# Kernel tuning notes

Hardware: AMD Instinct MI355X
Metric: run time of the kernel (lower is better)

## Reference

```python
import jax, jax.numpy as jnp
from jax import lax
import numpy as np

WIDTH = 3.0        # tool half-width (voxels)
SIGMA = 1.0        # soft mask edge (voxels)
BLUR_SIGMA = 1.5   # post-deposit isotropic blur sigma (voxels)
EPS = 1e-8


def _gauss_blur(x, sigma):
    """Separable Gaussian blur over the last two axes of x: [B, X, Y]."""
    radius = int(3 * sigma)
    t = jnp.arange(-radius, radius + 1, dtype=x.dtype)
    k = jnp.exp(-0.5 * (t / sigma) ** 2)
    k = k / k.sum()
    x4 = x[:, None]                      # [B,1,X,Y] NCHW
    kh = k.reshape(1, 1, -1, 1)
    x4 = lax.conv_general_dilated(x4, kh, (1, 1), 'SAME')
    kw = k.reshape(1, 1, 1, -1)
    x4 = lax.conv_general_dilated(x4, kw, (1, 1), 'SAME')
    return x4[:, 0]


def setup_inputs() -> dict:
    key = jax.random.key(0)
    k1, k2, k3 = jax.random.split(key, 3)
    B, H, W = 16, 1024, 1024
    occ = jax.random.uniform(k1, (B, H, W), dtype=jnp.float32)
    # push start/end points well inside the grid (voxel coordinates)
    action_start = jax.random.uniform(k2, (B, 3), minval=200.0, maxval=800.0, dtype=jnp.float32)
    action_end = action_start + jax.random.uniform(k3, (B, 3), minval=-150.0, maxval=150.0, dtype=jnp.float32)
    return {"occ": occ, "action_start": action_start, "action_end": action_end}


def reference(occ, action_start, action_end):
    # coordinate-convention transpose (see SplatPushModel docs)
    rho = jnp.swapaxes(occ, 1, 2)            # [B, X, Y]
    B, X, Y = rho.shape
    p0 = action_start[:, :2]                 # [B,2]
    p1 = action_end[:, :2]                   # [B,2]

    d = p1 - p0
    L = jnp.sqrt(jnp.sum(d * d, axis=-1) + EPS)      # [B] segment length
    u = d / L[:, None]                               # unit push direction
    n = jnp.stack([-u[:, 1], u[:, 0]], axis=-1)      # unit normal

    gx = jnp.arange(X, dtype=rho.dtype)[None, :, None]   # [1,X,1]
    gy = jnp.arange(Y, dtype=rho.dtype)[None, None, :]   # [1,1,Y]
    bc = lambda v: v[:, None, None]                      # [B] -> [B,1,1]

    # --- swept band: soft distance-to-segment mask ---
    rx = gx - bc(p0[:, 0])
    ry = gy - bc(p0[:, 1])
    t = jnp.clip(rx * bc(u[:, 0]) + ry * bc(u[:, 1]), 0.0, L[:, None, None])
    dx = rx - t * bc(u[:, 0])
    dy = ry - t * bc(u[:, 1])
    dist = jnp.sqrt(dx * dx + dy * dy + EPS)
    swept = jax.nn.sigmoid((WIDTH - dist) / SIGMA)       # [B,X,Y]

    m_swept = jnp.sum(rho * swept, axis=(1, 2))          # [B] mass to move
    pile_depth = m_swept / (2.0 * WIDTH)                 # [B]

    # --- landing zone probe (rectangle past p1) ---
    qx = gx - bc(p1[:, 0])
    qy = gy - bc(p1[:, 1])
    s = qx * bc(u[:, 0]) + qy * bc(u[:, 1])              # along-direction coord
    r = qx * bc(n[:, 0]) + qy * bc(n[:, 1])              # perpendicular coord
    lat = jax.nn.sigmoid((WIDTH - jnp.abs(r)) / SIGMA)
    probe = jax.nn.sigmoid(s / SIGMA) * jax.nn.sigmoid((bc(pile_depth) - s) / SIGMA) * lat
    existing = jnp.sum(rho * probe, axis=(1, 2))         # [B]
    extra = existing / (2.0 * WIDTH)                     # [B] forward extension

    # --- deposit band, shifted forward by extra_depth ---
    dep_mask = (jax.nn.sigmoid((s - bc(extra)) / SIGMA)
                * jax.nn.sigmoid((bc(extra) + bc(pile_depth) - s) / SIGMA)
                * lat)
    dep_norm = m_swept / (jnp.sum(dep_mask, axis=(1, 2)) + EPS)
    dep = dep_mask * dep_norm[:, None, None]             # mass-conserving deposit

    if BLUR_SIGMA > 0:
        dep = _gauss_blur(dep, BLUR_SIGMA)

    rho_new = rho * (1.0 - swept) + dep
    return jnp.swapaxes(rho_new, 1, 2)
```

## Files before the change

kernel.cpp:

```cpp
#include <hip/hip_runtime.h>
#include <hip/hip_bf16.h>
#include <math.h>

#define BB    16
#define HH    1024
#define WW    1024
#define NPIX  (HH * WW)
#define EPSF  1e-8f
#define RAD   4
#define MARG  24.f
#define NB1   128
#define NB2   64

struct BlurK { float k[9]; };

__device__ __forceinline__ float sigf(float z) {
    z = fmaxf(fminf(z, 40.f), -40.f);
    return 1.f / (1.f + __expf(-z));
}

struct Geom { float p0x, p0y, p1x, p1y, L, ux, uy; };

__device__ __forceinline__ Geom load_geom(const float* as, const float* ae, int b) {
    Geom g;
    g.p0x = as[3 * b];  g.p0y = as[3 * b + 1];
    g.p1x = ae[3 * b];  g.p1y = ae[3 * b + 1];
    float dx = g.p1x - g.p0x, dy = g.p1y - g.p0y;
    g.L  = sqrtf(dx * dx + dy * dy + EPSF);
    g.ux = dx / g.L;  g.uy = dy / g.L;
    return g;
}

__device__ __forceinline__ float sweptf(const Geom& g, float x, float y) {
    float rx = x - g.p0x, ry = y - g.p0y;
    float t  = fminf(fmaxf(rx * g.ux + ry * g.uy, 0.f), g.L);
    float dx = rx - t * g.ux, dy = ry - t * g.uy;
    float dist = sqrtf(dx * dx + dy * dy + EPSF);
    return sigf(3.f - dist);
}

__device__ __forceinline__ void slat(const Geom& g, float x, float y, float& s, float& lat) {
    float qx = x - g.p1x, qy = y - g.p1y;
    s = qx * g.ux + qy * g.uy;
    float r = qx * (-g.uy) + qy * g.ux;
    lat = sigf(3.f - fabsf(r));
}

__device__ __forceinline__ void capsule_bbox(const Geom& g, float m,
                                             int& x0, int& x1, int& y0, int& y1) {
    x0 = max(0, (int)floorf(fminf(g.p0x, g.p1x) - m));
    x1 = min(WW - 1, (int)ceilf(fmaxf(g.p0x, g.p1x) + m));
    y0 = max(0, (int)floorf(fminf(g.p0y, g.p1y) - m));
    y1 = min(HH - 1, (int)ceilf(fmaxf(g.p0y, g.p1y) + m));
}

__device__ __forceinline__ void strip_bbox(const Geom& g, float s0, float s1, float m,
                                           int& x0, int& x1, int& y0, int& y1) {
    float xmin = 1e9f, xmax = -1e9f, ymin = 1e9f, ymax = -1e9f;
    #pragma unroll
    for (int i = 0; i < 4; i++) {
        float s = (i & 1) ? s1 : s0;
        float r = (i & 2) ? m : -m;
        float x = g.p1x + s * g.ux - r * g.uy;
        float y = g.p1y + s * g.uy + r * g.ux;
        xmin = fminf(xmin, x); xmax = fmaxf(xmax, x);
        ymin = fminf(ymin, y); ymax = fmaxf(ymax, y);
    }
    x0 = max(0, (int)floorf(xmin)); x1 = min(WW - 1, (int)ceilf(xmax));
    y0 = max(0, (int)floorf(ymin)); y1 = min(HH - 1, (int)ceilf(ymax));
}

__device__ __forceinline__ float brb256(float v, float* sm) {
    #pragma unroll
    for (int off = 32; off > 0; off >>= 1) v += __shfl_down(v, off);
    const int lane = threadIdx.x & 63, wid = threadIdx.x >> 6;
    if (lane == 0) sm[wid] = v;
    __syncthreads();
    float r = sm[0] + sm[1] + sm[2] + sm[3];
    __syncthreads();
    return r;
}

__global__ __launch_bounds__(256)
void k_copy_mswept(const float* __restrict__ occ, const float* __restrict__ as,
                   const float* __restrict__ ae, float* __restrict__ out,
                   float* __restrict__ part1) {
    const int b = blockIdx.y, bx = blockIdx.x, tid = threadIdx.x;
    const float4* src = (const float4*)(occ + ((size_t)b << 20));
    float4*       dst = (float4*)(out + ((size_t)b << 20));
    const int base4 = bx * 2048 + tid;
    float4 v[8];
    #pragma unroll
    for (int k = 0; k < 8; k++) v[k] = src[base4 + k * 256];
    #pragma unroll
    for (int k = 0; k < 8; k++) dst[base4 + k * 256] = v[k];

    Geom g = load_geom(as, ae, b);
    int cx0, cx1, cy0, cy1; capsule_bbox(g, MARG, cx0, cx1, cy0, cy1);
    const int x = tid << 2;
    float sum = 0.f;
    if (x + 3 >= cx0 && x <= cx1) {
        #pragma unroll
        for (int k = 0; k < 8; k++) {
            const int y = bx * 8 + k;
            if (y >= cy0 && y <= cy1) {
                float fy = (float)y, fx = (float)x;
                sum += v[k].x * sweptf(g, fx + 0.f, fy);
                sum += v[k].y * sweptf(g, fx + 1.f, fy);
                sum += v[k].z * sweptf(g, fx + 2.f, fy);
                sum += v[k].w * sweptf(g, fx + 3.f, fy);
            }
        }
    }
    __shared__ float sm[4];
    float bs = brb256(sum, sm);
    if (tid == 0) part1[b * NB1 + bx] = bs;
}

__global__ __launch_bounds__(256)
void k_existing(const float* __restrict__ occ, const float* __restrict__ as,
                const float* __restrict__ ae, const float* __restrict__ part1,
                float* __restrict__ part2) {
    const int b = blockIdx.y, bx = blockIdx.x, tid = threadIdx.x;
    __shared__ float sm[4];
    const float m_swept = brb256((tid < NB1) ? part1[b * NB1 + tid] : 0.f, sm);
    const float pile = m_swept * (1.f / 6.f);

    Geom g = load_geom(as, ae, b);
    int x0, x1, y0, y1; strip_bbox(g, -MARG, pile + MARG, MARG, x0, x1, y0, y1);
    const float* base = occ + ((size_t)b << 20);
    float sum = 0.f;
    for (int y = y0 + bx; y <= y1; y += NB2) {
        float fy = (float)y;
        for (int x = x0 + tid; x <= x1; x += 256) {
            float s, lat; slat(g, (float)x, fy, s, lat);
            sum += base[((size_t)y << 10) + x] * sigf(s) * sigf(pile - s) * lat;
        }
    }
    float bs = brb256(sum, sm);
    if (tid == 0) part2[b * NB2 + bx] = bs;
}

__global__ __launch_bounds__(256)
void k_summask(const float* __restrict__ as, const float* __restrict__ ae,
               const float* __restrict__ part1, const float* __restrict__ part2,
               float* __restrict__ part3) {
    const int b = blockIdx.y, bx = blockIdx.x, tid = threadIdx.x;
    __shared__ float sm[4];
    const float m_swept  = brb256((tid < NB1) ? part1[b * NB1 + tid] : 0.f, sm);
    const float existing = brb256((tid < NB2) ? part2[b * NB2 + tid] : 0.f, sm);
    const float pile  = m_swept * (1.f / 6.f);
    const float extra = existing * (1.f / 6.f);

    Geom g = load_geom(as, ae, b);
    int x0, x1, y0, y1; strip_bbox(g, extra - MARG, extra + pile + MARG, MARG, x0, x1, y0, y1);
    float sum = 0.f;
    for (int y = y0 + bx; y <= y1; y += NB2) {
        float fy = (float)y;
        for (int x = x0 + tid; x <= x1; x += 256) {
            float s, lat; slat(g, (float)x, fy, s, lat);
            sum += sigf(s - extra) * sigf(extra + pile - s) * lat;
        }
    }
    float bs = brb256(sum, sm);
    if (tid == 0) part3[b * NB2 + bx] = bs;
}

#define TH 8
#define TW 128
__global__ __launch_bounds__(256)
void k_patch(const float* __restrict__ occ, const float* __restrict__ as,
             const float* __restrict__ ae, const float* __restrict__ part1,
             const float* __restrict__ part2, const float* __restrict__ part3,
             float* __restrict__ out, BlurK wk) {
    const int b = blockIdx.y, bx = blockIdx.x, tid = threadIdx.x;
    __shared__ float sm[4];
    const float m_swept  = brb256((tid < NB1) ? part1[b * NB1 + tid] : 0.f, sm);
    const float existing = brb256((tid < NB2) ? part2[b * NB2 + tid] : 0.f, sm);
    const float summask  = brb256((tid < NB2) ? part3[b * NB2 + tid] : 0.f, sm);
    const float pile     = m_swept * (1.f / 6.f);
    const float extra    = existing * (1.f / 6.f);
    const float dep_norm = m_swept / (summask + EPSF);

    Geom g = load_geom(as, ae, b);
    int cx0, cx1, cy0, cy1; capsule_bbox(g, MARG, cx0, cx1, cy0, cy1);
    int sx0, sx1, sy0, sy1; strip_bbox(g, extra - MARG, extra + pile + MARG, MARG, sx0, sx1, sy0, sy1);
    const int ux0 = min(cx0, sx0), ux1 = max(cx1, sx1);
    const int uy0 = min(cy0, sy0), uy1 = max(cy1, sy1);
    const int bw = ux1 - ux0 + 1, bh = uy1 - uy0 + 1;
    const int ntx = (bw + TW - 1) / TW, nty = (bh + TH - 1) / TH;

    __shared__ float draw[TH + 2 * RAD][TW + 2 * RAD];
    __shared__ float hb[TH + 2 * RAD][TW];
    const float* ob = occ + ((size_t)b << 20);
    float* outb = out + ((size_t)b << 20);

    for (int t = bx; t < ntx * nty; t += NB2) {
        const int tx = t % ntx, ty = t / ntx;
        const int xt = ux0 + tx * TW, yt = uy0 + ty * TH;
        for (int i = tid; i < (TH + 8) * (TW + 8); i += 256) {
            int ly = i / (TW + 8), lx = i % (TW + 8);
            int gy = yt - RAD + ly, gx = xt - RAD + lx;
            float v = 0.f;
            if (gx >= 0 && gx < WW && gy >= 0 && gy < HH) {
                float s, lat; slat(g, (float)gx, (float)gy, s, lat);
                v = sigf(s - extra) * sigf(extra + pile - s) * lat * dep_norm;
            }
            draw[ly][lx] = v;
        }
        __syncthreads();
        for (int i = tid; i < (TH + 8) * TW; i += 256) {
            int ly = i / TW, lx = i % TW;
            float acc = 0.f;
            #pragma unroll
            for (int j = 0; j < 9; j++) acc += wk.k[j] * draw[ly][lx + j];
            hb[ly][lx] = acc;
        }
        __syncthreads();
        for (int i = tid; i < TH * TW; i += 256) {
            int ly = i / TW, lx = i % TW;
            int gy = yt + ly, gx = xt + lx;
            if (gy < HH && gx < WW) {
                float acc = 0.f;
                #pragma unroll
                for (int j = 0; j < 9; j++) acc += wk.k[j] * hb[ly + j][lx];
                size_t off = ((size_t)gy << 10) + gx;
                float o = ob[off];
                outb[off] = o * (1.f - sweptf(g, (float)gx, (float)gy)) + acc;
            }
        }
        __syncthreads();
    }
}

extern "C" void kernel_launch(void* const* d_in, const int* in_sizes, int n_in,
                              void* d_out, int out_size, void* d_ws, size_t ws_size,
                              hipStream_t stream) {
    const float* occ = (const float*)d_in[0];
    const float* as  = (const float*)d_in[1];
    const float* ae  = (const float*)d_in[2];
    float* out   = (float*)d_out;
    float* part1 = (float*)d_ws;
    float* part2 = part1 + BB * NB1;
    float* part3 = part2 + BB * NB2;

    BlurK wk;
    {
        float s = 0.f;
        for (int i = 0; i < 9; i++) {
            float t = (float)(i - RAD) / 1.5f;
            wk.k[i] = expf(-0.5f * t * t);
            s += wk.k[i];
        }
        for (int i = 0; i < 9; i++) wk.k[i] /= s;
    }

    k_copy_mswept<<<dim3(NB1, BB), 256, 0, stream>>>(occ, as, ae, out, part1);
    k_existing   <<<dim3(NB2, BB), 256, 0, stream>>>(occ, as, ae, part1, part2);
    k_summask    <<<dim3(NB2, BB), 256, 0, stream>>>(as, ae, part1, part2, part3);
    k_patch      <<<dim3(NB2, BB), 256, 0, stream>>>(occ, as, ae, part1, part2, part3, out, wk);
}
```

Baseline: 142.8 us.

## Fuse scalar reductions into one kernel and merge copy with blurred deposit

The three per-batch scalar reductions (swept mass, existing mass, mask sum) move into a single kernel with one 1024-thread block per batch, computed sequentially within the block instead of across three launches with partial buffers. The copy pass and the patch pass are merged into one full-grid kernel: each block loads its 8 rows, applies the swept mask in registers, adds the blurred deposit strip computed in shared memory, and writes once. This removes the second read/write of the patch region and two launches. In exchange, the scalar kernel uses only 16 blocks, so it runs at low parallelism and sits serially before the main kernel. The fused kernel also needs more shared memory per block.

```diff
diff --git a/kernel.cpp b/kernel.cpp
--- a/kernel.cpp
+++ b/kernel.cpp
@@ -1,16 +1,14 @@
 #include <hip/hip_runtime.h>
-#include <hip/hip_bf16.h>
 #include <math.h>
 
 #define BB    16
 #define HH    1024
 #define WW    1024
-#define NPIX  (HH * WW)
 #define EPSF  1e-8f
 #define RAD   4
 #define MARG  24.f
-#define NB1   128
-#define NB2   64
+#define WMAX  256
+#define FW    (WMAX + 16)
 
 struct BlurK { float k[9]; };
 
@@ -70,167 +68,173 @@
     y0 = max(0, (int)floorf(ymin)); y1 = min(HH - 1, (int)ceilf(ymax));
 }
 
-__device__ __forceinline__ float brb256(float v, float* sm) {
+__device__ __forceinline__ float brb1024(float v, float* sm) {
     #pragma unroll
     for (int off = 32; off > 0; off >>= 1) v += __shfl_down(v, off);
     const int lane = threadIdx.x & 63, wid = threadIdx.x >> 6;
     if (lane == 0) sm[wid] = v;
     __syncthreads();
-    float r = sm[0] + sm[1] + sm[2] + sm[3];
+    float r = 0.f;
+    #pragma unroll
+    for (int i = 0; i < 16; i++) r += sm[i];
     __syncthreads();
     return r;
 }
 
+__global__ __launch_bounds__(1024)
+void k_scalars(const float* __restrict__ occ, const float* __restrict__ as,
+               const float* __restrict__ ae, float* __restrict__ sc) {
+    const int b = blockIdx.x, tid = threadIdx.x;
+    const int ty = tid >> 7, tx = tid & 127;
+    __shared__ float sm[16];
+    Geom g = load_geom(as, ae, b);
+    const float* base = occ + ((size_t)b << 20);
+
+    int x0, x1, y0, y1;
+    capsule_bbox(g, MARG, x0, x1, y0, y1);
+    float sum = 0.f;
+    for (int y = y0 + ty; y <= y1; y += 8) {
+        const float fy = (float)y;
+        for (int x = x0 + tx; x <= x1; x += 128)
+            sum += base[((size_t)y << 10) + x] * sweptf(g, (float)x, fy);
+    }
+    const float m_swept = brb1024(sum, sm);
+    const float pile = m_swept * (1.f / 6.f);
+
+    strip_bbox(g, -MARG, pile + MARG, MARG, x0, x1, y0, y1);
+    sum = 0.f;
+    for (int y = y0 + ty; y <= y1; y += 8) {
+        const float fy = (float)y;
+        for (int x = x0 + tx; x <= x1; x += 128) {
+            float s, lat; slat(g, (float)x, fy, s, lat);
+            sum += base[((size_t)y << 10) + x] * sigf(s) * sigf(pile - s) * lat;
+        }
+    }
+    const float existing = brb1024(sum, sm);
+    const float extra = existing * (1.f / 6.f);
+
+    strip_bbox(g, extra - MARG, extra + pile + MARG, MARG, x0, x1, y0, y1);
+    sum = 0.f;
+    for (int y = y0 + ty; y <= y1; y += 8) {
+        const float fy = (float)y;
+        for (int x = x0 + tx; x <= x1; x += 128) {
+            float s, lat; slat(g, (float)x, fy, s, lat);
+            sum += sigf(s - extra) * sigf(extra + pile - s) * lat;
+        }
+    }
+    const float summask = brb1024(sum, sm);
+
+    if (tid == 0) {
+        sc[b * 4 + 0] = pile;
+        sc[b * 4 + 1] = extra;
+        sc[b * 4 + 2] = m_swept / (summask + EPSF);
+    }
+}
+
 __global__ __launch_bounds__(256)
-void k_copy_mswept(const float* __restrict__ occ, const float* __restrict__ as,
-                   const float* __restrict__ ae, float* __restrict__ out,
-                   float* __restrict__ part1) {
+void k_fused(const float* __restrict__ occ, const float* __restrict__ as,
+             const float* __restrict__ ae, const float* __restrict__ sc,
+             float* __restrict__ out, BlurK wk) {
     const int b = blockIdx.y, bx = blockIdx.x, tid = threadIdx.x;
-    const float4* src = (const float4*)(occ + ((size_t)b << 20));
-    float4*       dst = (float4*)(out + ((size_t)b << 20));
+    const float pile     = sc[b * 4 + 0];
+    const float extra    = sc[b * 4 + 1];
+    const float dep_norm = sc[b * 4 + 2];
+    Geom g = load_geom(as, ae, b);
+
+    const size_t ibase = (size_t)b << 20;
+    const float4* src = (const float4*)(occ + ibase);
+    float4*       dst = (float4*)(out + ibase);
+    const int yb = bx * 8;
     const int base4 = bx * 2048 + tid;
+
     float4 v[8];
     #pragma unroll
     for (int k = 0; k < 8; k++) v[k] = src[base4 + k * 256];
-    #pragma unroll
-    for (int k = 0; k < 8; k++) dst[base4 + k * 256] = v[k];
-
-    Geom g = load_geom(as, ae, b);
+
     int cx0, cx1, cy0, cy1; capsule_bbox(g, MARG, cx0, cx1, cy0, cy1);
     const int x = tid << 2;
-    float sum = 0.f;
     if (x + 3 >= cx0 && x <= cx1) {
         #pragma unroll
         for (int k = 0; k < 8; k++) {
-            const int y = bx * 8 + k;
+            const int y = yb + k;
             if (y >= cy0 && y <= cy1) {
-                float fy = (float)y, fx = (float)x;
-                sum += v[k].x * sweptf(g, fx + 0.f, fy);
-                sum += v[k].y * sweptf(g, fx + 1.f, fy);
-                sum += v[k].z * sweptf(g, fx + 2.f, fy);
-                sum += v[k].w * sweptf(g, fx + 3.f, fy);
-            }
-        }
-    }
-    __shared__ float sm[4];
-    float bs = brb256(sum, sm);
-    if (tid == 0) part1[b * NB1 + bx] = bs;
-}
-
-__global__ __launch_bounds__(256)
-void k_existing(const float* __restrict__ occ, const float* __restrict__ as,
-                const float* __restrict__ ae, const float* __restrict__ part1,
-                float* __restrict__ part2) {
-    const int b = blockIdx.y, bx = blockIdx.x, tid = threadIdx.x;
-    __shared__ float sm[4];
-    const float m_swept = brb256((tid < NB1) ? part1[b * NB1 + tid] : 0.f, sm);
-    const float pile = m_swept * (1.f / 6.f);
-
-    Geom g = load_geom(as, ae, b);
-    int x0, x1, y0, y1; strip_bbox(g, -MARG, pile + MARG, MARG, x0, x1, y0, y1);
-    const float* base = occ + ((size_t)b << 20);
-    float sum = 0.f;
-    for (int y = y0 + bx; y <= y1; y += NB2) {
-        float fy = (float)y;
-        for (int x = x0 + tid; x <= x1; x += 256) {
-            float s, lat; slat(g, (float)x, fy, s, lat);
-            sum += base[((size_t)y << 10) + x] * sigf(s) * sigf(pile - s) * lat;
-        }
-    }
-    float bs = brb256(sum, sm);
-    if (tid == 0) part2[b * NB2 + bx] = bs;
-}
-
-__global__ __launch_bounds__(256)
-void k_summask(const float* __restrict__ as, const float* __restrict__ ae,
-               const float* __restrict__ part1, const float* __restrict__ part2,
-               float* __restrict__ part3) {
-    const int b = blockIdx.y, bx = blockIdx.x, tid = threadIdx.x;
-    __shared__ float sm[4];
-    const float m_swept  = brb256((tid < NB1) ? part1[b * NB1 + tid] : 0.f, sm);
-    const float existing = brb256((tid < NB2) ? part2[b * NB2 + tid] : 0.f, sm);
-    const float pile  = m_swept * (1.f / 6.f);
-    const float extra = existing * (1.f / 6.f);
-
-    Geom g = load_geom(as, ae, b);
-    int x0, x1, y0, y1; strip_bbox(g, extra - MARG, extra + pile + MARG, MARG, x0, x1, y0, y1);
-    float sum = 0.f;
-    for (int y = y0 + bx; y <= y1; y += NB2) {
-        float fy = (float)y;
-        for (int x = x0 + tid; x <= x1; x += 256) {
-            float s, lat; slat(g, (float)x, fy, s, lat);
-            sum += sigf(s - extra) * sigf(extra + pile - s) * lat;
-        }
-    }
-    float bs = brb256(sum, sm);
-    if (tid == 0) part3[b * NB2 + bx] = bs;
-}
-
-#define TH 8
-#define TW 128
-__global__ __launch_bounds__(256)
-void k_patch(const float* __restrict__ occ, const float* __restrict__ as,
-             const float* __restrict__ ae, const float* __restrict__ part1,
-             const float* __restrict__ part2, const float* __restrict__ part3,
-             float* __restrict__ out, BlurK wk) {
-    const int b = blockIdx.y, bx = blockIdx.x, tid = threadIdx.x;
-    __shared__ float sm[4];
-    const float m_swept  = brb256((tid < NB1) ? part1[b * NB1 + tid] : 0.f, sm);
-    const float existing = brb256((tid < NB2) ? part2[b * NB2 + tid] : 0.f, sm);
-    const float summask  = brb256((tid < NB2) ? part3[b * NB2 + tid] : 0.f, sm);
-    const float pile     = m_swept * (1.f / 6.f);
-    const float extra    = existing * (1.f / 6.f);
-    const float dep_norm = m_swept / (summask + EPSF);
-
-    Geom g = load_geom(as, ae, b);
-    int cx0, cx1, cy0, cy1; capsule_bbox(g, MARG, cx0, cx1, cy0, cy1);
-    int sx0, sx1, sy0, sy1; strip_bbox(g, extra - MARG, extra + pile + MARG, MARG, sx0, sx1, sy0, sy1);
-    const int ux0 = min(cx0, sx0), ux1 = max(cx1, sx1);
-    const int uy0 = min(cy0, sy0), uy1 = max(cy1, sy1);
-    const int bw = ux1 - ux0 + 1, bh = uy1 - uy0 + 1;
-    const int ntx = (bw + TW - 1) / TW, nty = (bh + TH - 1) / TH;
-
-    __shared__ float draw[TH + 2 * RAD][TW + 2 * RAD];
-    __shared__ float hb[TH + 2 * RAD][TW];
-    const float* ob = occ + ((size_t)b << 20);
-    float* outb = out + ((size_t)b << 20);
-
-    for (int t = bx; t < ntx * nty; t += NB2) {
-        const int tx = t % ntx, ty = t / ntx;
-        const int xt = ux0 + tx * TW, yt = uy0 + ty * TH;
-        for (int i = tid; i < (TH + 8) * (TW + 8); i += 256) {
-            int ly = i / (TW + 8), lx = i % (TW + 8);
-            int gy = yt - RAD + ly, gx = xt - RAD + lx;
-            float v = 0.f;
-            if (gx >= 0 && gx < WW && gy >= 0 && gy < HH) {
-                float s, lat; slat(g, (float)gx, (float)gy, s, lat);
-                v = sigf(s - extra) * sigf(extra + pile - s) * lat * dep_norm;
-            }
-            draw[ly][lx] = v;
-        }
-        __syncthreads();
-        for (int i = tid; i < (TH + 8) * TW; i += 256) {
-            int ly = i / TW, lx = i % TW;
-            float acc = 0.f;
-            #pragma unroll
-            for (int j = 0; j < 9; j++) acc += wk.k[j] * draw[ly][lx + j];
-            hb[ly][lx] = acc;
-        }
-        __syncthreads();
-        for (int i = tid; i < TH * TW; i += 256) {
-            int ly = i / TW, lx = i % TW;
-            int gy = yt + ly, gx = xt + lx;
-            if (gy < HH && gx < WW) {
-                float acc = 0.f;
-                #pragma unroll
-                for (int j = 0; j < 9; j++) acc += wk.k[j] * hb[ly + j][lx];
-                size_t off = ((size_t)gy << 10) + gx;
-                float o = ob[off];
-                outb[off] = o * (1.f - sweptf(g, (float)gx, (float)gy)) + acc;
-            }
-        }
-        __syncthreads();
-    }
+                const float fy = (float)y, fx = (float)x;
+                v[k].x *= 1.f - sweptf(g, fx + 0.f, fy);
+                v[k].y *= 1.f - sweptf(g, fx + 1.f, fy);
+                v[k].z *= 1.f - sweptf(g, fx + 2.f, fy);
+                v[k].w *= 1.f - sweptf(g, fx + 3.f, fy);
+            }
+        }
+    }
+
+    int sx0, sx1, sy0, sy1;
+    strip_bbox(g, extra - MARG, extra + pile + MARG, MARG, sx0, sx1, sy0, sy1);
+
+    __shared__ float draw[16][FW];
+    __shared__ float hb[16][WMAX];
+
+    if (yb + 7 >= sy0 && yb <= sy1) {
+        const int cxa = sx0 & ~3;
+        for (int cx = cxa; cx <= sx1; cx += WMAX) {
+            const int w = min(WMAX, sx1 - cx + 1);
+
+            for (int i = tid; i < 16 * FW; i += 256) {
+                const int ly = i / FW, lx = i - ly * FW;
+                if (lx < w + 8) {
+                    const int gy = yb - 4 + ly, gx = cx - 4 + lx;
+                    float val = 0.f;
+                    if ((unsigned)gx < WW && (unsigned)gy < HH) {
+                        float s, lat; slat(g, (float)gx, (float)gy, s, lat);
+                        val = sigf(s - extra) * sigf(extra + pile - s) * lat * dep_norm;
+                    }
+                    draw[ly][lx] = val;
+                }
+            }
+            __syncthreads();
+
+            for (int i = tid; i < 16 * WMAX; i += 256) {
+                const int ly = i >> 8, lx = i & 255;
+                if (lx < w) {
+                    float acc = 0.f;
+                    #pragma unroll
+                    for (int j = 0; j < 9; j++) acc += wk.k[j] * draw[ly][lx + j];
+                    hb[ly][lx] = acc;
+                }
+            }
+            __syncthreads();
+
+            for (int i = tid; i < 8 * WMAX; i += 256) {
+                const int k = i >> 8, lx = i & 255;
+                if (lx < w) {
+                    float acc = 0.f;
+                    #pragma unroll
+                    for (int j = 0; j < 9; j++) acc += wk.k[j] * hb[k + j][lx];
+                    draw[k][lx] = acc;
+                }
+            }
+            __syncthreads();
+
+            const int lx0 = (tid << 2) - cx;
+            if (lx0 >= 0 && lx0 < w) {
+                if (lx0 + 3 < w) {
+                    #pragma unroll
+                    for (int k = 0; k < 8; k++) {
+                        const float4 vb = *(const float4*)&draw[k][lx0];
+                        v[k].x += vb.x; v[k].y += vb.y; v[k].z += vb.z; v[k].w += vb.w;
+                    }
+                } else {
+                    #pragma unroll
+                    for (int k = 0; k < 8; k++)
+                        for (int e = 0; e < 4; e++)
+                            if (lx0 + e < w) (&v[k].x)[e] += draw[k][lx0 + e];
+                }
+            }
+            __syncthreads();
+        }
+    }
+
+    #pragma unroll
+    for (int k = 0; k < 8; k++) dst[base4 + k * 256] = v[k];
 }
 
 extern "C" void kernel_launch(void* const* d_in, const int* in_sizes, int n_in,
@@ -239,10 +243,8 @@
     const float* occ = (const float*)d_in[0];
     const float* as  = (const float*)d_in[1];
     const float* ae  = (const float*)d_in[2];
-    float* out   = (float*)d_out;
-    float* part1 = (float*)d_ws;
-    float* part2 = part1 + BB * NB1;
-    float* part3 = part2 + BB * NB2;
+    float* out = (float*)d_out;
+    float* sc  = (float*)d_ws;
 
     BlurK wk;
     {
@@ -255,8 +257,6 @@
         for (int i = 0; i < 9; i++) wk.k[i] /= s;
     }
 
-    k_copy_mswept<<<dim3(NB1, BB), 256, 0, stream>>>(occ, as, ae, out, part1);
-    k_existing   <<<dim3(NB2, BB), 256, 0, stream>>>(occ, as, ae, part1, part2);
-    k_summask    <<<dim3(NB2, BB), 256, 0, stream>>>(as, ae, part1, part2, part3);
-    k_patch      <<<dim3(NB2, BB), 256, 0, stream>>>(occ, as, ae, part1, part2, part3, out, wk);
-}
+    k_scalars<<<dim3(BB), 1024, 0, stream>>>(occ, as, ae, sc);
+    k_fused  <<<dim3(HH / 8, BB), 256, 0, stream>>>(occ, as, ae, sc, out, wk);
+}
```

Result: slower. 167.0 us (+17.0%).
